# Performance work log

Hardware: AMD Instinct MI355X
Metric: run time of the kernel (lower is better)

Reference implementation:

```python
import jax, jax.numpy as jnp
import numpy as np

D_MODEL = 1024
NUM_HEADS = 16
D_K = D_MODEL // NUM_HEADS


def setup_inputs() -> dict:
    key = jax.random.key(0)
    ks = jax.random.split(key, 11)
    B, S = 2, 2048
    scale = 1.0 / np.sqrt(D_MODEL)
    inp = {
        'q': jax.random.normal(ks[0], (B, S, D_MODEL), dtype=jnp.float32),
        'k': jax.random.normal(ks[1], (B, S, D_MODEL), dtype=jnp.float32),
        'v': jax.random.normal(ks[2], (B, S, D_MODEL), dtype=jnp.float32),
        'W_q': jax.random.normal(ks[3], (D_MODEL, D_MODEL), dtype=jnp.float32) * scale,
        'b_q': jnp.zeros((D_MODEL,), dtype=jnp.float32),
        'W_k': jax.random.normal(ks[4], (D_MODEL, D_MODEL), dtype=jnp.float32) * scale,
        'b_k': jnp.zeros((D_MODEL,), dtype=jnp.float32),
        'W_v': jax.random.normal(ks[5], (D_MODEL, D_MODEL), dtype=jnp.float32) * scale,
        'b_v': jnp.zeros((D_MODEL,), dtype=jnp.float32),
        'W_o': jax.random.normal(ks[6], (D_MODEL, D_MODEL), dtype=jnp.float32) * scale,
        'b_o': jnp.zeros((D_MODEL,), dtype=jnp.float32),
    }
    return inp


def _split_heads(x):
    # [B, S, D] -> [B, H, S, d_k]
    B, S, _ = x.shape
    return x.reshape(B, S, NUM_HEADS, D_K).transpose(0, 2, 1, 3)


def reference(q, k, v, W_q, b_q, W_k, b_k, W_v, b_v, W_o, b_o):
    # Linear projections (torch Linear: x @ W.T + b)
    qh = _split_heads(q @ W_q.T + b_q)  # [B,H,S,dk]
    kh = _split_heads(k @ W_k.T + b_k)
    vh = _split_heads(v @ W_v.T + b_v)
    scores = jnp.einsum('bhsd,bhtd->bhst', qh, kh) / jnp.sqrt(
        jnp.asarray(D_K, dtype=qh.dtype))  # [B,H,S,S]
    probs = jax.nn.softmax(scores, axis=-1)
    attn = jnp.einsum('bhst,bhtd->bhsd', probs, vh)  # [B,H,S,dk]
    B, H, S, dk = attn.shape
    combined = attn.transpose(0, 2, 1, 3).reshape(B, S, H * dk)  # [B,S,D]
    return combined @ W_o.T + b_o
```

## Files before the change

kernel.cpp:

```cpp
#include <hip/hip_runtime.h>
#include <hip/hip_bf16.h>

typedef __bf16 bf16;
typedef __attribute__((ext_vector_type(4))) __bf16 bf16x4;
typedef __attribute__((ext_vector_type(8))) __bf16 bf16x8;
typedef __attribute__((ext_vector_type(4))) float f32x4;

#define AS1C(p) ((const __attribute__((address_space(1))) void*)(p))
#define AS3(p)  ((__attribute__((address_space(3))) void*)(p))

static constexpr int B_ = 2, S_ = 2048, DM = 1024, H_ = 16, DK = 64;
static constexpr int M_ = B_ * S_;
static constexpr int NW = DM * DM;
static constexpr float QSCL = 0.125f * 1.44269504088896340736f;

__device__ __forceinline__ float fast_exp2(float x) {
#if __has_builtin(__builtin_amdgcn_exp2f)
  return __builtin_amdgcn_exp2f(x);
#else
  return exp2f(x);
#endif
}

__global__ __launch_bounds__(256) void cast_w4(
    const float* Wq, const float* Wk, const float* Wv, const float* Wo,
    bf16* Wc, bf16* WoC)
{
  const int z = blockIdx.y;
  const float* in = z == 0 ? Wq : (z == 1 ? Wk : (z == 2 ? Wv : Wo));
  const float s = z == 0 ? QSCL : 1.0f;
  bf16* out = z < 3 ? (Wc + (size_t)z * NW) : WoC;
  const int i = (blockIdx.x * 256 + threadIdx.x) * 8;
  f32x4 a = *(const f32x4*)(in + i);
  f32x4 b = *(const f32x4*)(in + i + 4);
  bf16x8 o;
#pragma unroll
  for (int j = 0; j < 4; ++j) { o[j] = (bf16)(a[j] * s); o[4 + j] = (bf16)(b[j] * s); }
  *(bf16x8*)(out + i) = o;
}

template<int WTM, bool A_BF16, bool OUT_F32>
__device__ __forceinline__ void gemm_body(
    const void* __restrict__ Ain, const bf16* __restrict__ W,
    const float* __restrict__ bias, float bscale, void* __restrict__ Cout,
    bool transv, int M, int N, int K, int bx, int by)
{
  constexpr int BMt = 2 * WTM;
  constexpr int WI  = WTM / 16;
  __shared__ bf16 As[2 * BMt * 32];
  __shared__ bf16 Bs[2 * 128 * 32];

  const int tid  = threadIdx.x;
  const int wave = tid >> 6, lane = tid & 63;
  const int quad = lane >> 4, l16 = lane & 15;
  const int wm = wave >> 1, wn = wave & 1;
  const int row0 = by * BMt;
  const int col0 = bx * 128;

  const int srow  = lane >> 2;
  const int skcol = (lane & 3) * 8;

  const int arow  = (tid >> 1) & (BMt - 1);
  const int ak16  = (tid & 1) * 16;
  const float* agp = nullptr;
  f32x4 pre[8];
  if constexpr (!A_BF16) {
    agp = (const float*)Ain + (size_t)(row0 + arow) * K + ak16;
#pragma unroll
    for (int hf = 0; hf < 2; ++hf)
#pragma unroll
      for (int c = 0; c < 4; ++c)
        pre[hf * 4 + c] = *(const f32x4*)(agp + hf * 32 + c * 4);
  }

  f32x4 acc[WI][4] = {};

  for (int k0 = 0; k0 < K; k0 += 64) {
    __syncthreads();
    if constexpr (A_BF16) {
      const bf16* A = (const bf16*)Ain;
#pragma unroll
      for (int hf = 0; hf < 2; ++hf)
#pragma unroll
        for (int c = wave; c < BMt / 16; c += 4)
          __builtin_amdgcn_global_load_lds(
              AS1C(A + (size_t)(row0 + c * 16 + srow) * K + k0 + hf * 32 + skcol),
              AS3(As + hf * BMt * 32 + c * 16 * 32), 16, 0, 0);
    } else {
#pragma unroll
      for (int hf = 0; hf < 2; ++hf) {
        bf16x8 w0, w1;
#pragma unroll
        for (int j = 0; j < 4; ++j) {
          w0[j]     = (bf16)pre[hf * 4 + 0][j];
          w0[4 + j] = (bf16)pre[hf * 4 + 1][j];
          w1[j]     = (bf16)pre[hf * 4 + 2][j];
          w1[4 + j] = (bf16)pre[hf * 4 + 3][j];
        }
        bf16* dst = As + hf * BMt * 32 + arow * 32 + ak16;
        *(bf16x8*)dst = w0;
        *(bf16x8*)(dst + 8) = w1;
      }
    }
#pragma unroll
    for (int hf = 0; hf < 2; ++hf)
#pragma unroll
      for (int i = 0; i < 2; ++i) {
        const int c = wave * 2 + i;
        __builtin_amdgcn_global_load_lds(
            AS1C(W + (size_t)(col0 + c * 16 + srow) * K + k0 + hf * 32 + skcol),
            AS3(Bs + hf * 128 * 32 + c * 16 * 32), 16, 0, 0);
      }
    __syncthreads();

    if constexpr (!A_BF16) {
      if (k0 + 64 < K) {
#pragma unroll
        for (int hf = 0; hf < 2; ++hf)
#pragma unroll
          for (int c = 0; c < 4; ++c)
            pre[hf * 4 + c] = *(const f32x4*)(agp + k0 + 64 + hf * 32 + c * 4);
      }
    }

#pragma unroll
    for (int hf = 0; hf < 2; ++hf) {
      bf16x8 a[WI], bfr[4];
#pragma unroll
      for (int i = 0; i < WI; ++i)
        a[i] = *(const bf16x8*)(As + hf * BMt * 32 + (wm * WTM + i * 16 + l16) * 32 + quad * 8);
#pragma unroll
      for (int j = 0; j < 4; ++j)
        bfr[j] = *(const bf16x8*)(Bs + hf * 128 * 32 + (wn * 64 + j * 16 + l16) * 32 + quad * 8);
#pragma unroll
      for (int i = 0; i < WI; ++i)
#pragma unroll
        for (int j = 0; j < 4; ++j)
          acc[i][j] = __builtin_amdgcn_mfma_f32_16x16x32_bf16(a[i], bfr[j], acc[i][j], 0, 0, 0);
    }
  }

#pragma unroll
  for (int j = 0; j < 4; ++j) {
    const int col = col0 + wn * 64 + j * 16 + l16;
    const float bv = bias[col] * bscale;
    if (!OUT_F32 && transv) {
      const int hh = col >> 6, dd = col & 63;
#pragma unroll
      for (int i = 0; i < WI; ++i) {
        const int row = row0 + wm * WTM + i * 16 + quad * 4;
        const int bb2 = row >> 11, tok = row & 2047;
        bf16x4 o;
#pragma unroll
        for (int r = 0; r < 4; ++r) o[r] = (bf16)(acc[i][j][r] + bv);
        *(bf16x4*)((bf16*)Cout + (((size_t)bb2 * H_ + hh) * DK + dd) * S_ + tok) = o;
      }
    } else {
#pragma unroll
      for (int i = 0; i < WI; ++i) {
#pragma unroll
        for (int r = 0; r < 4; ++r) {
          const int row = row0 + wm * WTM + i * 16 + quad * 4 + r;
          const float val = acc[i][j][r] + bv;
          if constexpr (OUT_F32)
            ((float*)Cout)[(size_t)row * N + col] = val;
          else
            ((bf16*)Cout)[(size_t)row * N + col] = (bf16)val;
        }
      }
    }
  }
}

__global__ __launch_bounds__(256) void gemm_qkv(
    const float* A0, const float* A1, const float* A2,
    const bf16* __restrict__ Wc,
    const float* b0, const float* b1, const float* b2,
    bf16* C0, bf16* C1, bf16* C2, int M, int N, int K)
{
  const int id = blockIdx.x;
  const int z  = id >> 8;
  const int r  = id & 255;
  const int by = r & 31;
  const int bx = r >> 5;
  const float* A = z == 0 ? A0 : (z == 1 ? A1 : A2);
  const float* bias = z == 0 ? b0 : (z == 1 ? b1 : b2);
  const float bscale = z == 0 ? QSCL : 1.0f;
  bf16* C = z == 0 ? C0 : (z == 1 ? C1 : C2);
  gemm_body<64, false, false>(A, Wc + (size_t)z * NW, bias, bscale, C,
                              z == 2, M, N, K, bx, by);
}

__global__ __launch_bounds__(256) void gemm_out(
    const bf16* __restrict__ Ain, const bf16* __restrict__ W,
    const float* __restrict__ bias, float* __restrict__ Cout,
    int M, int N, int K)
{
  const int id = blockIdx.x;
  const int by = id & 63;
  const int bx = id >> 6;
  gemm_body<32, true, true>(Ain, W, bias, 1.0f, Cout, false, M, N, K, bx, by);
}

__global__ __launch_bounds__(256) void attn_kernel(
    const bf16* Q, const bf16* __restrict__ Kb,
    const bf16* __restrict__ Vtg, bf16* O)
{
  __shared__ bf16 Kt[64 * 72];
  __shared__ bf16 Vt[64 * 72];
  __shared__ bf16 Ps[4 * 32 * 72];

  const int tid  = threadIdx.x;
  const int wave = tid >> 6, lane = tid & 63;
  const int quad = lane >> 4, l16 = lane & 15;
  const int id = blockIdx.x;
  const int hb = id & 31;
  const int h = hb & 15, b = hb >> 4;
  const int qt = id >> 5;
  const int qA = qt * 128 + wave * 32;
  const size_t base  = (size_t)b * S_ * DM + (size_t)h * DK;
  const size_t baseV = ((size_t)b * H_ + h) * DK * S_;

  bf16x8 qf[2][2];
#pragma unroll
  for (int f = 0; f < 2; ++f)
#pragma unroll
    for (int kt = 0; kt < 2; ++kt)
      qf[f][kt] = *(const bf16x8*)(Q + base + (size_t)(qA + f * 16 + l16) * DM + kt * 32 + quad * 8);

  const bool kside = (wave < 2);
  const int srow  = kside ? (tid >> 1) : ((tid - 128) >> 1);
  const int shalf = tid & 1;
  const bf16* gp = kside
      ? (Kb + base + (size_t)srow * DM + shalf * 32)
      : (Vtg + baseV + (size_t)srow * S_ + shalf * 32);
  const size_t gstep = kside ? (size_t)64 * DM : 64;
  bf16* ldst = (kside ? Kt : Vt) + srow * 72 + shalf * 32;

  bf16x8 st[4];
#pragma unroll
  for (int c = 0; c < 4; ++c) st[c] = *(const bf16x8*)(gp + c * 8);
  gp += gstep;

  f32x4 lacc[2] = {};
  f32x4 accO[2][4] = {};
  bf16* Pw = Ps + wave * 32 * 72;

  constexpr int NIT = S_ / 64;
  for (int it = 0; it < NIT; ++it) {
    __syncthreads();
#pragma unroll
    for (int c = 0; c < 4; ++c) *(bf16x8*)(ldst + c * 8) = st[c];
    __syncthreads();

    if (it + 1 < NIT) {
#pragma unroll
      for (int c = 0; c < 4; ++c) st[c] = *(const bf16x8*)(gp + c * 8);
      gp += gstep;
    }

    f32x4 sc[2][4];
#pragma unroll
    for (int ct = 0; ct < 4; ++ct) {
      const bf16* kp = Kt + (ct * 16 + l16) * 72 + quad * 8;
      const bf16x8 kf0 = *(const bf16x8*)kp;
      const bf16x8 kf1 = *(const bf16x8*)(kp + 32);
#pragma unroll
      for (int f = 0; f < 2; ++f) {
        f32x4 a = {0.f, 0.f, 0.f, 0.f};
        a = __builtin_amdgcn_mfma_f32_16x16x32_bf16(kf0, qf[f][0], a, 0, 0, 0);
        a = __builtin_amdgcn_mfma_f32_16x16x32_bf16(kf1, qf[f][1], a, 0, 0, 0);
        sc[f][ct] = a;
      }
    }

#pragma unroll
    for (int f = 0; f < 2; ++f)
#pragma unroll
      for (int ct = 0; ct < 4; ++ct) {
        bf16x4 pk;
#pragma unroll
        for (int r = 0; r < 4; ++r) {
          const float p = fast_exp2(sc[f][ct][r]);
          lacc[f][r] += p;
          pk[r] = (bf16)p;
        }
        *(bf16x4*)(Pw + (f * 16 + l16) * 72 + ct * 16 + quad * 4) = pk;
      }

    bf16x8 pf[2][2];
#pragma unroll
    for (int f = 0; f < 2; ++f) {
      pf[f][0] = *(const bf16x8*)(Pw + (f * 16 + l16) * 72 + quad * 8);
      pf[f][1] = *(const bf16x8*)(Pw + (f * 16 + l16) * 72 + 32 + quad * 8);
    }

#pragma unroll
    for (int dt = 0; dt < 4; ++dt) {
      const bf16* vp = Vt + (dt * 16 + l16) * 72;
      const bf16x8 vf0 = *(const bf16x8*)(vp + quad * 8);
      const bf16x8 vf1 = *(const bf16x8*)(vp + 32 + quad * 8);
#pragma unroll
      for (int f = 0; f < 2; ++f) {
        accO[f][dt] = __builtin_amdgcn_mfma_f32_16x16x32_bf16(vf0, pf[f][0], accO[f][dt], 0, 0, 0);
        accO[f][dt] = __builtin_amdgcn_mfma_f32_16x16x32_bf16(vf1, pf[f][1], accO[f][dt], 0, 0, 0);
      }
    }
  }

#pragma unroll
  for (int f = 0; f < 2; ++f) {
    float l_s = (lacc[f][0] + lacc[f][1]) + (lacc[f][2] + lacc[f][3]);
    l_s += __shfl_xor(l_s, 16, 64);
    l_s += __shfl_xor(l_s, 32, 64);
    const float inv = 1.0f / l_s;
#pragma unroll
    for (int dt = 0; dt < 4; ++dt) {
      bf16x4 o;
#pragma unroll
      for (int r = 0; r < 4; ++r) o[r] = (bf16)(accO[f][dt][r] * inv);
      *(bf16x4*)(O + base + (size_t)(qA + f * 16 + l16) * DM + dt * 16 + quad * 4) = o;
    }
  }
}

extern "C" void kernel_launch(void* const* d_in, const int* in_sizes, int n_in,
                              void* d_out, int out_size, void* d_ws, size_t ws_size,
                              hipStream_t stream) {
  (void)in_sizes; (void)n_in; (void)out_size; (void)ws_size;
  const float* q  = (const float*)d_in[0];
  const float* k  = (const float*)d_in[1];
  const float* v  = (const float*)d_in[2];
  const float* Wq = (const float*)d_in[3];
  const float* bq = (const float*)d_in[4];
  const float* Wk = (const float*)d_in[5];
  const float* bk = (const float*)d_in[6];
  const float* Wv = (const float*)d_in[7];
  const float* bvv= (const float*)d_in[8];
  const float* Wo = (const float*)d_in[9];
  const float* bo = (const float*)d_in[10];
  float* out = (float*)d_out;

  char* ws = (char*)d_ws;
  const size_t MB = 1024 * 1024;
  bf16* Qb  = (bf16*)(ws);
  bf16* Kbf = (bf16*)(ws + 8 * MB);
  bf16* Vtg = (bf16*)(ws + 16 * MB);
  bf16* Wc  = (bf16*)(ws + 24 * MB);
  bf16* WoC = (bf16*)(ws + 30 * MB);
  bf16* Ab  = Qb;

  dim3 bb(256, 1, 1);

  cast_w4<<<dim3(NW / 2048, 4, 1), bb, 0, stream>>>(Wq, Wk, Wv, Wo, Wc, WoC);

  gemm_qkv<<<dim3(768, 1, 1), bb, 0, stream>>>(
      q, k, v, Wc, bq, bk, bvv, Qb, Kbf, Vtg, M_, DM, DM);

  attn_kernel<<<dim3(512, 1, 1), bb, 0, stream>>>(Qb, Kbf, Vtg, Ab);

  gemm_out<<<dim3(512, 1, 1), bb, 0, stream>>>(Ab, WoC, bo, out, M_, DM, DM);
}
```

Measured before the change: 224.2 us.

## Double-buffer K/V tiles, swizzle LDS, keep P in registers for PV MFMA

The attention kernel now double-buffers the K and V tiles in shared memory, so there is one barrier per iteration instead of two, and the next tile is stored while the current one is consumed. Shared-memory rows use an XOR swizzle instead of padding. The P tile no longer round-trips through LDS: the probabilities stay in registers and feed 16x16x16 bf16 MFMAs directly. The PV product now uses twice as many smaller MFMA instructions, and shared memory grows for the double buffers.

```diff
diff --git a/kernel.cpp b/kernel.cpp
--- a/kernel.cpp
+++ b/kernel.cpp
@@ -5,6 +5,7 @@
 typedef __attribute__((ext_vector_type(4))) __bf16 bf16x4;
 typedef __attribute__((ext_vector_type(8))) __bf16 bf16x8;
 typedef __attribute__((ext_vector_type(4))) float f32x4;
+typedef __attribute__((ext_vector_type(4))) short short4v;
 
 #define AS1C(p) ((const __attribute__((address_space(1))) void*)(p))
 #define AS3(p)  ((__attribute__((address_space(3))) void*)(p))
@@ -19,6 +20,17 @@
   return __builtin_amdgcn_exp2f(x);
 #else
   return exp2f(x);
+#endif
+}
+
+__device__ __forceinline__ f32x4 mfma_pv(bf16x4 a, bf16x4 b, f32x4 c) {
+#if __has_builtin(__builtin_amdgcn_mfma_f32_16x16x16_bf16)
+  return __builtin_amdgcn_mfma_f32_16x16x16_bf16(a, b, c, 0, 0, 0);
+#else
+  union U { bf16x4 h; short4v s; };
+  U ua; ua.h = a;
+  U ub; ub.h = b;
+  return __builtin_amdgcn_mfma_f32_16x16x16bf16_1k(ua.s, ub.s, c, 0, 0, 0);
 #endif
 }
 
@@ -206,9 +218,8 @@
     const bf16* Q, const bf16* __restrict__ Kb,
     const bf16* __restrict__ Vtg, bf16* O)
 {
-  __shared__ bf16 Kt[64 * 72];
-  __shared__ bf16 Vt[64 * 72];
-  __shared__ bf16 Ps[4 * 32 * 72];
+  __shared__ bf16 Kt[2 * 64 * 64];
+  __shared__ bf16 Vt[2 * 64 * 64];
 
   const int tid  = threadIdx.x;
   const int wave = tid >> 6, lane = tid & 63;
@@ -235,36 +246,38 @@
       ? (Kb + base + (size_t)srow * DM + shalf * 32)
       : (Vtg + baseV + (size_t)srow * S_ + shalf * 32);
   const size_t gstep = kside ? (size_t)64 * DM : 64;
-  bf16* ldst = (kside ? Kt : Vt) + srow * 72 + shalf * 32;
+  char* sb = (char*)(kside ? (void*)Kt : (void*)Vt) + srow * 128;
+  const int sw_s = (srow & 7) << 4;
 
   bf16x8 st[4];
 #pragma unroll
   for (int c = 0; c < 4; ++c) st[c] = *(const bf16x8*)(gp + c * 8);
   gp += gstep;
+#pragma unroll
+  for (int c = 0; c < 4; ++c)
+    *(bf16x8*)(sb + ((shalf * 64 + c * 16) ^ sw_s)) = st[c];
+#pragma unroll
+  for (int c = 0; c < 4; ++c) st[c] = *(const bf16x8*)(gp + c * 8);
+  gp += gstep;
 
   f32x4 lacc[2] = {};
   f32x4 accO[2][4] = {};
-  bf16* Pw = Ps + wave * 32 * 72;
+  const int sw = (l16 & 7) << 4;
+
+  __syncthreads();
 
   constexpr int NIT = S_ / 64;
   for (int it = 0; it < NIT; ++it) {
-    __syncthreads();
-#pragma unroll
-    for (int c = 0; c < 4; ++c) *(bf16x8*)(ldst + c * 8) = st[c];
-    __syncthreads();
-
-    if (it + 1 < NIT) {
-#pragma unroll
-      for (int c = 0; c < 4; ++c) st[c] = *(const bf16x8*)(gp + c * 8);
-      gp += gstep;
-    }
+    const int cur = it & 1, nxt = cur ^ 1;
+    const char* Kc = (const char*)Kt + cur * 8192;
+    const char* Vc = (const char*)Vt + cur * 8192;
 
     f32x4 sc[2][4];
 #pragma unroll
     for (int ct = 0; ct < 4; ++ct) {
-      const bf16* kp = Kt + (ct * 16 + l16) * 72 + quad * 8;
-      const bf16x8 kf0 = *(const bf16x8*)kp;
-      const bf16x8 kf1 = *(const bf16x8*)(kp + 32);
+      const char* kp = Kc + (ct * 16 + l16) * 128;
+      const bf16x8 kf0 = *(const bf16x8*)(kp + ((quad * 16) ^ sw));
+      const bf16x8 kf1 = *(const bf16x8*)(kp + ((64 + quad * 16) ^ sw));
 #pragma unroll
       for (int f = 0; f < 2; ++f) {
         f32x4 a = {0.f, 0.f, 0.f, 0.f};
@@ -274,38 +287,42 @@
       }
     }
 
+    if (it + 1 < NIT) {
+#pragma unroll
+      for (int c = 0; c < 4; ++c)
+        *(bf16x8*)(sb + nxt * 8192 + ((shalf * 64 + c * 16) ^ sw_s)) = st[c];
+      if (it + 2 < NIT) {
+#pragma unroll
+        for (int c = 0; c < 4; ++c) st[c] = *(const bf16x8*)(gp + c * 8);
+        gp += gstep;
+      }
+    }
+
+    bf16x4 pk[2][4];
 #pragma unroll
     for (int f = 0; f < 2; ++f)
 #pragma unroll
-      for (int ct = 0; ct < 4; ++ct) {
-        bf16x4 pk;
+      for (int ct = 0; ct < 4; ++ct)
 #pragma unroll
         for (int r = 0; r < 4; ++r) {
           const float p = fast_exp2(sc[f][ct][r]);
           lacc[f][r] += p;
-          pk[r] = (bf16)p;
+          pk[f][ct][r] = (bf16)p;
         }
-        *(bf16x4*)(Pw + (f * 16 + l16) * 72 + ct * 16 + quad * 4) = pk;
-      }
-
-    bf16x8 pf[2][2];
-#pragma unroll
-    for (int f = 0; f < 2; ++f) {
-      pf[f][0] = *(const bf16x8*)(Pw + (f * 16 + l16) * 72 + quad * 8);
-      pf[f][1] = *(const bf16x8*)(Pw + (f * 16 + l16) * 72 + 32 + quad * 8);
-    }
 
 #pragma unroll
     for (int dt = 0; dt < 4; ++dt) {
-      const bf16* vp = Vt + (dt * 16 + l16) * 72;
-      const bf16x8 vf0 = *(const bf16x8*)(vp + quad * 8);
-      const bf16x8 vf1 = *(const bf16x8*)(vp + 32 + quad * 8);
-#pragma unroll
-      for (int f = 0; f < 2; ++f) {
-        accO[f][dt] = __builtin_amdgcn_mfma_f32_16x16x32_bf16(vf0, pf[f][0], accO[f][dt], 0, 0, 0);
-        accO[f][dt] = __builtin_amdgcn_mfma_f32_16x16x32_bf16(vf1, pf[f][1], accO[f][dt], 0, 0, 0);
-      }
-    }
+      const char* vp = Vc + (dt * 16 + l16) * 128;
+#pragma unroll
+      for (int ct = 0; ct < 4; ++ct) {
+        const bf16x4 vf = *(const bf16x4*)(vp + ((ct * 32 + quad * 8) ^ sw));
+#pragma unroll
+        for (int f = 0; f < 2; ++f)
+          accO[f][dt] = mfma_pv(vf, pk[f][ct], accO[f][dt]);
+      }
+    }
+
+    __syncthreads();
   }
 
 #pragma unroll
```

After: 222.3 us. About the same (-0.9%).
